# Kernel optimization log

Hardware: AMD Instinct MI355X
Metric: run time of the kernel (lower is better)

## Reference

```python
import jax, jax.numpy as jnp
from jax import lax
import numpy as np

D_MODEL = 96; D_STATE = 16; SSM_RATIO = 2.0; D_CONV = 3; K = 4
D_INNER = int(SSM_RATIO * D_MODEL)      # 192
DT_RANK = -(-D_MODEL // 16)             # ceil(96/16) = 6
B_SZ = 4; H = 32; W = 32

# ---- zig-zag (snake) index helpers (static numpy) ----
def _snake_h(Hh, Ww):
    idx = np.tile(np.arange(Ww), (Hh, 1)); idx[1::2] = idx[1::2, ::-1]; return idx  # (H,W)

def _snake_v(Hh, Ww):
    idx = np.tile(np.arange(Hh)[:, None], (1, Ww)); idx[:, 1::2] = idx[::-1, 1::2]; return idx  # (H,W)

def _h_scan(x, d):
    Hh, Ww = x.shape[-2:]
    if d == 'left':
        x = jnp.flip(x, (-1, -2))
    return x[:, :, np.arange(Hh)[:, None], _snake_h(Hh, Ww)]

def _v_scan(x, d):
    Bb, Cc, Hh, Ww = x.shape
    if d == 'up':
        x = jnp.flip(x, (-1, -2))
    t = x[:, :, _snake_v(Hh, Ww), np.arange(Ww)[None, :]]  # gather along H per column
    return jnp.swapaxes(t, -1, -2).reshape(Bb, Cc, Hh, Ww)

def _h_merge(x, d):
    Hh, Ww = x.shape[-2:]
    t = x[:, :, np.arange(Hh)[:, None], _snake_h(Hh, Ww)]
    if d == 'left':
        t = jnp.flip(t, (-1, -2))
    return t

def _v_merge(x, d):
    Hh, Ww = x.shape[-2:]
    t2 = jnp.swapaxes(x, -1, -2)  # (B,C,W,H); requires H==W like the torch source
    t = t2[:, :, _snake_v(Hh, Ww), np.arange(Ww)[None, :]]
    if d == 'up':
        t = jnp.flip(t, (-1, -2))
    return t

def cross_scan(x):
    return jnp.stack([_v_scan(x, 'down'), _v_scan(x, 'up'), _h_scan(x, 'right'), _h_scan(x, 'left')], axis=1)

def cross_merge(ys):
    return (_v_merge(ys[:, 0], 'down') + _v_merge(ys[:, 1], 'up')
            + _h_merge(ys[:, 2], 'right') + _h_merge(ys[:, 3], 'left'))

def selective_scan(u, delta, A, Bs, Cs, Dp, delta_bias):
    # u,delta:(B,K,D,L)  A:(K,D,N)  Bs,Cs:(B,K,N,L)  Dp,delta_bias:(K,D)
    delta = jax.nn.softplus(delta + delta_bias[None, :, :, None])
    dA = jnp.exp(jnp.einsum('bkdl,kdn->lbkdn', delta, A))
    dBu = jnp.einsum('bkdl,bkdl,bknl->lbkdn', delta, u, Bs)
    Ct = jnp.moveaxis(Cs, -1, 0)  # (L,B,K,N)
    def step(h, inp):
        dA_t, dBu_t, c_t = inp
        h = dA_t * h + dBu_t
        return h, jnp.einsum('bkdn,bkn->bkd', h, c_t)
    h0 = jnp.zeros(dA.shape[1:], u.dtype)
    _, ys = lax.scan(step, h0, (dA, dBu, Ct))
    return jnp.moveaxis(ys, 0, -1) + Dp[None, :, :, None] * u  # (B,K,D,L)

def setup_inputs() -> dict:
    key = jax.random.key(0)
    ks = jax.random.split(key, 8)
    x = jax.random.normal(ks[0], (B_SZ, D_MODEL, H, W), jnp.float32)
    in_proj_w = jax.random.normal(ks[1], (2 * D_INNER, D_MODEL), jnp.float32) * (D_MODEL ** -0.5)
    conv_w = jax.random.normal(ks[2], (D_INNER, 1, D_CONV, D_CONV), jnp.float32) * 0.2  # depthwise
    conv_b = jnp.zeros((D_INNER,), jnp.float32)
    x_proj_w = jax.random.normal(ks[3], (K, DT_RANK + 2 * D_STATE, D_INNER), jnp.float32) * (D_INNER ** -0.5)
    s = DT_RANK ** -0.5
    dt_w = jax.random.uniform(ks[4], (K, D_INNER, DT_RANK), jnp.float32, -s, s)
    dt = jax.random.uniform(ks[5], (K, D_INNER), jnp.float32, 0.001, 0.1)
    dt_b = jnp.log(jnp.expm1(dt))  # inverse softplus, as in dt_init
    A_logs = jnp.tile(jnp.log(jnp.arange(1, D_STATE + 1, dtype=jnp.float32)), (K * D_INNER, 1))
    Ds = jnp.ones((K * D_INNER,), jnp.float32)
    gn_gamma = jnp.ones((D_INNER,), jnp.float32)
    gn_beta = jnp.zeros((D_INNER,), jnp.float32)
    out_proj_w = jax.random.normal(ks[6], (D_MODEL, D_INNER), jnp.float32) * (D_INNER ** -0.5)
    return {'x': x, 'in_proj_w': in_proj_w, 'conv_w': conv_w, 'conv_b': conv_b,
            'x_proj_w': x_proj_w, 'dt_w': dt_w, 'dt_b': dt_b, 'A_logs': A_logs, 'Ds': Ds,
            'gn_gamma': gn_gamma, 'gn_beta': gn_beta, 'out_proj_w': out_proj_w}

def reference(x, in_proj_w, conv_w, conv_b, x_proj_w, dt_w, dt_b, A_logs, Ds, gn_gamma, gn_beta, out_proj_w):
    Bb, _, Hh, Ww = x.shape; L = Hh * Ww
    xz = jnp.einsum('bchw,oc->bohw', x, in_proj_w)          # in_proj (1x1 conv, no bias)
    xx, z = jnp.split(xz, 2, axis=1)
    z = jax.nn.silu(z)
    xx = lax.conv_general_dilated(xx, conv_w, (1, 1), 'SAME', feature_group_count=D_INNER,
                                  dimension_numbers=('NCHW', 'OIHW', 'NCHW')) + conv_b[None, :, None, None]
    xx = jax.nn.silu(xx)
    xs = cross_scan(xx).reshape(Bb, K, D_INNER, L)          # 4-direction zig-zag scan
    x_dbl = jnp.einsum('bkdl,kcd->bkcl', xs, x_proj_w)
    dts = jnp.einsum('bkrl,kdr->bkdl', x_dbl[:, :, :DT_RANK], dt_w)
    Bs = x_dbl[:, :, DT_RANK:DT_RANK + D_STATE]
    Cs = x_dbl[:, :, DT_RANK + D_STATE:]
    A = -jnp.exp(A_logs).reshape(K, D_INNER, D_STATE)
    y = selective_scan(xs, dts, A, Bs, Cs, Ds.reshape(K, D_INNER), dt_b)
    y = cross_merge(y.reshape(Bb, K, D_INNER, Hh, Ww))       # (B,D,H,W)
    # out_norm: GroupNorm(1, d_inner) == layernorm over (C,H,W) per sample
    mu = jnp.mean(y, axis=(1, 2, 3), keepdims=True)
    var = jnp.var(y, axis=(1, 2, 3), keepdims=True)
    y = (y - mu) * lax.rsqrt(var + 1e-6)
    y = y * gn_gamma[None, :, None, None] + gn_beta[None, :, None, None]
    y = y * z
    return jnp.einsum('bchw,oc->bohw', y, out_proj_w)
```

## Files before the change

### kernel.cpp

```cpp
#include <hip/hip_runtime.h>
#include <math.h>

#define Bsz 4
#define DM 96
#define DI 192
#define NS 16
#define RK 6
#define KK 4
#define HH 32
#define WW 32
#define LL 1024
#define NC 64
#define CS 16

__device__ __forceinline__ float silu_f(float x) { return x / (1.f + __expf(-x)); }

__device__ __forceinline__ int l_of_hw(int k, int h, int w) {
    if (k == 1 || k == 3) { h = 31 - h; w = 31 - w; }
    if (k < 2) return w * 32 + ((w & 1) ? 31 - h : h);
    return h * 32 + ((h & 1) ? 31 - w : w);
}

__global__ void in_proj_k(const float* __restrict__ x, const float* __restrict__ w,
                          float* __restrict__ xx, float* __restrict__ zs,
                          float* __restrict__ stats) {
    int bi = blockIdx.x;
    int t = threadIdx.x;
    if (bi == 0 && t < 2 * Bsz) stats[t] = 0.f;
    int lb = bi & 3;
    int og = (bi >> 2) % 48;
    int b = bi / 192;
    int l = lb * 256 + t;
    const float* xb = x + (size_t)b * DM * LL + l;
    float acc[8];
#pragma unroll
    for (int g = 0; g < 8; g++) acc[g] = 0.f;
    for (int c = 0; c < DM; c++) {
        float xv = xb[(size_t)c * LL];
#pragma unroll
        for (int g = 0; g < 8; g++)
            acc[g] = fmaf(xv, w[(size_t)(og * 8 + g) * DM + c], acc[g]);
    }
#pragma unroll
    for (int g = 0; g < 8; g++) {
        int o = og * 8 + g;
        if (o < DI) xx[((size_t)b * DI + o) * LL + l] = acc[g];
        else        zs[((size_t)b * DI + (o - DI)) * LL + l] = silu_f(acc[g]);
    }
}

__global__ void convxs_k(const float* __restrict__ xx, const float* __restrict__ cw,
                         const float* __restrict__ cb, float* __restrict__ xs) {
    __shared__ float tile[32][65];
    int bi = blockIdx.x;
    int h0 = bi % 32;
    int dt = (bi / 32) % 3;
    int b = bi / 96;
    int d0 = dt * 64;
    int t = threadIdx.x;
    int wi = t & 31, dg = t >> 5;

#pragma unroll
    for (int pass = 0; pass < 8; pass++) {
        int di = pass * 8 + dg;
        int d = d0 + di;
        const float* xp = xx + ((size_t)b * DI + d) * LL;
        const float* wp = cw + d * 9;
        float acc = cb[d];
#pragma unroll
        for (int kh = 0; kh < 3; kh++) {
            int hh = h0 + kh - 1;
            if (hh < 0 || hh >= HH) continue;
#pragma unroll
            for (int kw = 0; kw < 3; kw++) {
                int ww2 = wi + kw - 1;
                if (ww2 < 0 || ww2 >= WW) continue;
                acc = fmaf(xp[hh * WW + ww2], wp[kh * 3 + kw], acc);
            }
        }
        tile[wi][di] = silu_f(acc);
    }
    __syncthreads();

    int di = t & 63, hg = t >> 6;
#pragma unroll
    for (int k = 0; k < KK; k++) {
        float* xsk = xs + ((size_t)b * KK + k) * LL * DI;
#pragma unroll
        for (int rep = 0; rep < 8; rep++) {
            int w2 = rep * 4 + hg;
            int l = l_of_hw(k, h0, w2);
            xsk[(size_t)l * DI + d0 + di] = tile[w2][di];
        }
    }
}

__global__ void __launch_bounds__(512)
xdbl_k(const float* __restrict__ xs, const float* __restrict__ xpw,
       float* __restrict__ xdbl) {
    __shared__ float tile[64 * 193];
    int blk = blockIdx.x;
    int bk = blk >> 4, lt = blk & 15;
    int k = bk & 3;
    int t = threadIdx.x;

    const float4* src4 = (const float4*)(xs + ((size_t)bk * LL + lt * 64) * DI);
#pragma unroll
    for (int i = 0; i < 6; i++) {
        int j4 = t + i * 512;
        float4 v = src4[j4];
        int l = j4 / 48;
        int d = (j4 % 48) * 4;
        float* dst = &tile[l * 193 + d];
        dst[0] = v.x; dst[1] = v.y; dst[2] = v.z; dst[3] = v.w;
    }
    __syncthreads();

    int ll = t & 63;
    int cg = t >> 6;
    int c0 = cg * 5;
    int wlim = (c0 + 5 <= 38) ? 5 : (38 - c0);
    const float* wk = xpw + (size_t)k * 38 * DI;

    float acc[5];
#pragma unroll
    for (int j = 0; j < 5; j++) acc[j] = 0.f;
    const float* xrow = &tile[ll * 193];
#pragma unroll 4
    for (int d = 0; d < DI; d++) {
        float xv = xrow[d];
#pragma unroll
        for (int j = 0; j < 5; j++) {
            int cc = c0 + j; cc = (cc > 37) ? 37 : cc;
            acc[j] = fmaf(xv, wk[(size_t)cc * DI + d], acc[j]);
        }
    }
    float* orow = xdbl + ((size_t)bk * LL + lt * 64 + ll) * 38;
#pragma unroll
    for (int j = 0; j < 5; j++)
        if (j < wlim) orow[c0 + j] = acc[j];
}

__global__ void scan_p1(const float* __restrict__ xs, const float* __restrict__ xdbl,
                        const float* __restrict__ dtw_g, const float* __restrict__ dtb_g,
                        const float* __restrict__ Alog,
                        float* __restrict__ Pst, float* __restrict__ Hloc) {
    int blk = blockIdx.x;
    int bk = blk / NC, c = blk % NC;
    int k = bk & 3;
    int d = threadIdx.x;
    int kd = k * DI + d;

    float A[NS];
#pragma unroll
    for (int n = 0; n < NS; n++) A[n] = -__expf(Alog[(size_t)kd * NS + n]);
    float dtw[RK];
#pragma unroll
    for (int r = 0; r < RK; r++) dtw[r] = dtw_g[(size_t)kd * RK + r];
    float dtb = dtb_g[kd];

    float h[NS], P[NS];
#pragma unroll
    for (int n = 0; n < NS; n++) { h[n] = 0.f; P[n] = 1.f; }

    const float* xdbase = xdbl + ((size_t)bk * LL + c * CS) * 38;
    const float* xsbase = xs + ((size_t)bk * LL + c * CS) * DI;

    for (int s = 0; s < CS; s++) {
        const float* xd = xdbase + s * 38;
        float dt = dtb;
#pragma unroll
        for (int r = 0; r < RK; r++) dt = fmaf(xd[r], dtw[r], dt);
        dt = (dt > 20.f) ? dt : log1pf(__expf(dt));
        float du = dt * xsbase[(size_t)s * DI + d];
#pragma unroll
        for (int n = 0; n < NS; n++) {
            float a = __expf(dt * A[n]);
            h[n] = fmaf(a, h[n], du * xd[6 + n]);
            P[n] *= a;
        }
    }
    size_t base = ((size_t)blk * DI + d) * NS;
#pragma unroll
    for (int n = 0; n < NS; n++) { Pst[base + n] = P[n]; Hloc[base + n] = h[n]; }
}

__global__ void scan_mid(const float* __restrict__ Pst, float* __restrict__ Hloc) {
    int gid = blockIdx.x * 256 + threadIdx.x;
    int bk = gid / (DI * NS);
    int dn = gid % (DI * NS);
    size_t base = (size_t)bk * NC * DI * NS + dn;
    float h = 0.f;
    for (int c = 0; c < NC; c++) {
        size_t a = base + (size_t)c * DI * NS;
        float p = Pst[a];
        float loc = Hloc[a];
        Hloc[a] = h;
        h = fmaf(p, h, loc);
    }
}

__global__ void scan_p3(const float* __restrict__ xs, const float* __restrict__ xdbl,
                        const float* __restrict__ dtw_g, const float* __restrict__ dtb_g,
                        const float* __restrict__ Alog, const float* __restrict__ Ds,
                        const float* __restrict__ Hin, float* __restrict__ ys) {
    int blk = blockIdx.x;
    int bk = blk / NC, c = blk % NC;
    int k = bk & 3;
    int d = threadIdx.x;
    int kd = k * DI + d;

    float A[NS];
#pragma unroll
    for (int n = 0; n < NS; n++) A[n] = -__expf(Alog[(size_t)kd * NS + n]);
    float dtw[RK];
#pragma unroll
    for (int r = 0; r < RK; r++) dtw[r] = dtw_g[(size_t)kd * RK + r];
    float dtb = dtb_g[kd];
    float Dp = Ds[kd];

    float h[NS];
    size_t hbase = ((size_t)blk * DI + d) * NS;
#pragma unroll
    for (int n = 0; n < NS; n++) h[n] = Hin[hbase + n];

    const float* xdbase = xdbl + ((size_t)bk * LL + c * CS) * 38;
    const float* xsbase = xs + ((size_t)bk * LL + c * CS) * DI;
    float* ybase = ys + ((size_t)bk * LL + c * CS) * DI;

    for (int s = 0; s < CS; s++) {
        const float* xd = xdbase + s * 38;
        float dt = dtb;
#pragma unroll
        for (int r = 0; r < RK; r++) dt = fmaf(xd[r], dtw[r], dt);
        dt = (dt > 20.f) ? dt : log1pf(__expf(dt));
        float u = xsbase[(size_t)s * DI + d];
        float du = dt * u;
        float y = 0.f;
#pragma unroll
        for (int n = 0; n < NS; n++) {
            float a = __expf(dt * A[n]);
            h[n] = fmaf(a, h[n], du * xd[6 + n]);
            y = fmaf(h[n], xd[22 + n], y);
        }
        ybase[(size_t)s * DI + d] = fmaf(Dp, u, y);
    }
}

#define MT 16
__global__ void merge_k(const float* __restrict__ ys, float* __restrict__ ym,
                        float* __restrict__ stats) {
    __shared__ float tile[MT][DI + 1];
    __shared__ float sh1[3], sh2[3];
    int b = blockIdx.y;
    int hw0 = blockIdx.x * MT;
    int d = threadIdx.x;
    const float* yb = ys + (size_t)b * KK * LL * DI;

    float s1 = 0.f, s2 = 0.f;
#pragma unroll
    for (int hwi = 0; hwi < MT; hwi++) {
        int hw = hw0 + hwi;
        int h = hw >> 5, w = hw & 31;
        int l0 = l_of_hw(0, h, w);
        int l1 = l_of_hw(1, h, w);
        int l2 = l_of_hw(2, h, w);
        int l3 = l_of_hw(3, h, w);
        float v = yb[((size_t)0 * LL + l0) * DI + d]
                + yb[((size_t)1 * LL + l1) * DI + d]
                + yb[((size_t)2 * LL + l2) * DI + d]
                + yb[((size_t)3 * LL + l3) * DI + d];
        tile[hwi][d] = v;
        s1 += v; s2 = fmaf(v, v, s2);
    }
#pragma unroll
    for (int off = 32; off > 0; off >>= 1) {
        s1 += __shfl_down(s1, off);
        s2 += __shfl_down(s2, off);
    }
    int lane = threadIdx.x & 63, wid = threadIdx.x >> 6;
    if (lane == 0) { sh1[wid] = s1; sh2[wid] = s2; }
    __syncthreads();
    if (threadIdx.x == 0) {
        atomicAdd(&stats[b * 2],     sh1[0] + sh1[1] + sh1[2]);
        atomicAdd(&stats[b * 2 + 1], sh2[0] + sh2[1] + sh2[2]);
    }
#pragma unroll
    for (int rep = 0; rep < MT; rep++) {
        int j = rep * DI + threadIdx.x;
        int d2 = j >> 4;
        int hwi = j & (MT - 1);
        ym[((size_t)b * DI + d2) * LL + hw0 + hwi] = tile[hwi][d2];
    }
}

__global__ void yz_k(const float* __restrict__ ym, const float* __restrict__ zs,
                     const float* __restrict__ g, const float* __restrict__ be,
                     const float* __restrict__ stats, float* __restrict__ yz) {
    int idx = blockIdx.x * 256 + threadIdx.x;
    int c = (idx >> 10) % DI;
    int b = idx / (LL * DI);
    const float Ninv = 1.f / (float)(DI * LL);
    float mu = stats[b * 2] * Ninv;
    float var = stats[b * 2 + 1] * Ninv - mu * mu;
    float rstd = rsqrtf(var + 1e-6f);
    float v = (ym[idx] - mu) * rstd * g[c] + be[c];
    yz[idx] = v * zs[idx];
}

__global__ void out_k(const float* __restrict__ yz, const float* __restrict__ wo,
                      float* __restrict__ out) {
    int bi = blockIdx.x;
    int t = threadIdx.x;
    int lb = bi & 3;
    int og = (bi >> 2) % 24;
    int b = bi / 96;
    int l = lb * 256 + t;
    const float* yb = yz + (size_t)b * DI * LL + l;
    float acc[4];
#pragma unroll
    for (int g = 0; g < 4; g++) acc[g] = 0.f;
    for (int c = 0; c < DI; c++) {
        float yv = yb[(size_t)c * LL];
#pragma unroll
        for (int g = 0; g < 4; g++)
            acc[g] = fmaf(yv, wo[(size_t)(og * 4 + g) * DI + c], acc[g]);
    }
#pragma unroll
    for (int g = 0; g < 4; g++)
        out[((size_t)b * DM + og * 4 + g) * LL + l] = acc[g];
}

extern "C" void kernel_launch(void* const* d_in, const int* in_sizes, int n_in,
                              void* d_out, int out_size, void* d_ws, size_t ws_size,
                              hipStream_t stream) {
    const float* x    = (const float*)d_in[0];
    const float* ipw  = (const float*)d_in[1];
    const float* cw   = (const float*)d_in[2];
    const float* cb   = (const float*)d_in[3];
    const float* xpw  = (const float*)d_in[4];
    const float* dtw  = (const float*)d_in[5];
    const float* dtb  = (const float*)d_in[6];
    const float* Alog = (const float*)d_in[7];
    const float* Ds   = (const float*)d_in[8];
    const float* gng  = (const float*)d_in[9];
    const float* gnb  = (const float*)d_in[10];
    const float* opw  = (const float*)d_in[11];
    float* out = (float*)d_out;

    float* ws = (float*)d_ws;
    const size_t o_xx   = 0;
    const size_t o_zs   = o_xx + (size_t)Bsz * DI * LL;
    const size_t o_xs   = o_zs + (size_t)Bsz * DI * LL;
    const size_t o_xdbl = o_xs + (size_t)Bsz * KK * LL * DI;
    const size_t o_P    = o_xdbl + (size_t)Bsz * KK * LL * 38;
    const size_t o_H    = o_P + (size_t)Bsz * KK * NC * DI * NS;
    const size_t o_st   = o_H + (size_t)Bsz * KK * NC * DI * NS;

    float* xx    = ws + o_xx;
    float* zs    = ws + o_zs;
    float* xs    = ws + o_xs;
    float* xdbl  = ws + o_xdbl;
    float* Pst   = ws + o_P;
    float* Hst   = ws + o_H;
    float* stats = ws + o_st;
    float* ys = Pst;
    float* ym = xx;
    float* yz = Hst;

    hipLaunchKernelGGL(in_proj_k, dim3(768), dim3(256), 0, stream, x, ipw, xx, zs, stats);
    hipLaunchKernelGGL(convxs_k, dim3(384), dim3(256), 0, stream, xx, cw, cb, xs);
    hipLaunchKernelGGL(xdbl_k, dim3(256), dim3(512), 0, stream, xs, xpw, xdbl);
    hipLaunchKernelGGL(scan_p1, dim3(Bsz * KK * NC), dim3(192), 0, stream,
                       xs, xdbl, dtw, dtb, Alog, Pst, Hst);
    hipLaunchKernelGGL(scan_mid, dim3(192), dim3(256), 0, stream, Pst, Hst);
    hipLaunchKernelGGL(scan_p3, dim3(Bsz * KK * NC), dim3(192), 0, stream,
                       xs, xdbl, dtw, dtb, Alog, Ds, Hst, ys);
    hipLaunchKernelGGL(merge_k, dim3(LL / MT, Bsz), dim3(192), 0, stream, ys, ym, stats);
    hipLaunchKernelGGL(yz_k, dim3(3072), dim3(256), 0, stream, ym, zs, gng, gnb, stats, yz);
    hipLaunchKernelGGL(out_k, dim3(384), dim3(256), 0, stream, yz, opw, out);
}
```

Baseline: 233.7 us.

## Fuse all stages into one cooperative persistent kernel with grid syncs

Replaces the chain of nine kernel launches with a single cooperative kernel of 512 blocks that runs each stage in turn, separated by grid-wide barriers. Stages are re-partitioned to fit the fixed grid: in_proj computes 12 outputs per thread, xdbl streams xs through a smaller LDS slice, scan blocks each handle two chunks, and the yz normalisation is fused into the out-projection. The aim is to remove per-launch overhead and the intermediate yz round trip to memory. In exchange, several stages now run with fewer or idle threads, and each grid sync adds its own cost. The old multi-kernel path stays as a fallback if the cooperative launch fails.

```diff
diff --git a/kernel.cpp b/kernel.cpp
--- a/kernel.cpp
+++ b/kernel.cpp
@@ -1,5 +1,8 @@
 #include <hip/hip_runtime.h>
+#include <hip/hip_cooperative_groups.h>
 #include <math.h>
+
+namespace cg = cooperative_groups;
 
 #define Bsz 4
 #define DM 96
@@ -12,6 +15,7 @@
 #define LL 1024
 #define NC 64
 #define CS 16
+#define MT 8
 
 __device__ __forceinline__ float silu_f(float x) { return x / (1.f + __expf(-x)); }
 
@@ -19,6 +23,327 @@
     if (k == 1 || k == 3) { h = 31 - h; w = 31 - w; }
     if (k < 2) return w * 32 + ((w & 1) ? 31 - h : h);
     return h * 32 + ((h & 1) ? 31 - w : w);
+}
+
+#define O_XX   0
+#define O_ZS   (O_XX + Bsz * DI * LL)
+#define O_XS   (O_ZS + Bsz * DI * LL)
+#define O_XDBL (O_XS + Bsz * KK * LL * DI)
+#define O_P    (O_XDBL + Bsz * KK * LL * 38)
+#define O_H    (O_P + Bsz * KK * NC * DI * NS)
+#define O_ST   (O_H + Bsz * KK * NC * DI * NS)
+
+__global__ void __launch_bounds__(256, 2)
+mega_k(const float* __restrict__ x, const float* __restrict__ ipw,
+       const float* __restrict__ cw, const float* __restrict__ cb,
+       const float* __restrict__ xpw, const float* __restrict__ dtw_g,
+       const float* __restrict__ dtb_g, const float* __restrict__ Alog,
+       const float* __restrict__ Ds, const float* __restrict__ gng,
+       const float* __restrict__ gnb, const float* __restrict__ opw,
+       float* __restrict__ out, float* __restrict__ ws) {
+    cg::grid_group grid = cg::this_grid();
+    __shared__ float lds[3136];
+
+    float* xx    = ws + O_XX;
+    float* zs    = ws + O_ZS;
+    float* xs    = ws + O_XS;
+    float* xdbl  = ws + O_XDBL;
+    float* Pst   = ws + O_P;
+    float* Hst   = ws + O_H;
+    float* stats = ws + O_ST;
+    float* ys = Pst;
+    float* ym = xx;
+
+    int bi = blockIdx.x;
+    int t = threadIdx.x;
+
+    {
+        if (bi == 0 && t < 2 * Bsz) stats[t] = 0.f;
+        int b = bi / 128;
+        int rest = bi % 128;
+        int og = rest >> 2;
+        int lb = rest & 3;
+        int l = lb * 256 + t;
+        const float* xb = x + (size_t)b * DM * LL + l;
+        float acc[12];
+#pragma unroll
+        for (int g = 0; g < 12; g++) acc[g] = 0.f;
+        for (int c = 0; c < DM; c++) {
+            float xv = xb[(size_t)c * LL];
+#pragma unroll
+            for (int g = 0; g < 12; g++)
+                acc[g] = fmaf(xv, ipw[(size_t)(og * 12 + g) * DM + c], acc[g]);
+        }
+#pragma unroll
+        for (int g = 0; g < 12; g++) {
+            int o = og * 12 + g;
+            if (o < DI) xx[((size_t)b * DI + o) * LL + l] = acc[g];
+            else        zs[((size_t)b * DI + (o - DI)) * LL + l] = silu_f(acc[g]);
+        }
+    }
+    grid.sync();
+
+    if (bi < 384) {
+        float (*tile)[65] = (float(*)[65])lds;
+        int h0 = bi % 32;
+        int dt = (bi / 32) % 3;
+        int b = bi / 96;
+        int d0 = dt * 64;
+        int wi = t & 31, dg = t >> 5;
+#pragma unroll
+        for (int pass = 0; pass < 8; pass++) {
+            int di = pass * 8 + dg;
+            int d = d0 + di;
+            const float* xp = xx + ((size_t)b * DI + d) * LL;
+            const float* wp = cw + d * 9;
+            float acc = cb[d];
+#pragma unroll
+            for (int kh = 0; kh < 3; kh++) {
+                int hh = h0 + kh - 1;
+                if (hh < 0 || hh >= HH) continue;
+#pragma unroll
+                for (int kw = 0; kw < 3; kw++) {
+                    int ww2 = wi + kw - 1;
+                    if (ww2 < 0 || ww2 >= WW) continue;
+                    acc = fmaf(xp[hh * WW + ww2], wp[kh * 3 + kw], acc);
+                }
+            }
+            tile[wi][di] = silu_f(acc);
+        }
+        __syncthreads();
+        int di = t & 63, hg = t >> 6;
+#pragma unroll
+        for (int k = 0; k < KK; k++) {
+            float* xsk = xs + ((size_t)b * KK + k) * LL * DI;
+#pragma unroll
+            for (int rep = 0; rep < 8; rep++) {
+                int w2 = rep * 4 + hg;
+                int l = l_of_hw(k, h0, w2);
+                xsk[(size_t)l * DI + d0 + di] = tile[w2][di];
+            }
+        }
+    }
+    grid.sync();
+
+    if (bi < 256) {
+        int bk = bi >> 4, lt = bi & 15;
+        int k = bk & 3;
+        int ll = t & 63;
+        int cgp = t >> 6;
+        int c0 = cgp * 10;
+        int wlim = 38 - c0; if (wlim > 10) wlim = 10;
+        const float* wk = xpw + (size_t)k * 38 * DI;
+        const float4* src4 = (const float4*)(xs + ((size_t)bk * LL + lt * 64) * DI);
+        float acc[10];
+#pragma unroll
+        for (int j = 0; j < 10; j++) acc[j] = 0.f;
+#pragma unroll
+        for (int sl = 0; sl < 4; sl++) {
+            __syncthreads();
+#pragma unroll
+            for (int i = 0; i < 3; i++) {
+                int j = t + i * 256;
+                int l = j / 12;
+                int c4 = j % 12;
+                float4 v = src4[(size_t)l * 48 + sl * 12 + c4];
+                float* dst = &lds[l * 49 + c4 * 4];
+                dst[0] = v.x; dst[1] = v.y; dst[2] = v.z; dst[3] = v.w;
+            }
+            __syncthreads();
+            const float* xrow = &lds[ll * 49];
+            const float* wks = wk + sl * 48;
+#pragma unroll 4
+            for (int dd = 0; dd < 48; dd++) {
+                float xv = xrow[dd];
+#pragma unroll
+                for (int j = 0; j < 10; j++) {
+                    int cc = c0 + j; cc = (cc > 37) ? 37 : cc;
+                    acc[j] = fmaf(xv, wks[(size_t)cc * DI + dd], acc[j]);
+                }
+            }
+        }
+        float* orow = xdbl + ((size_t)bk * LL + lt * 64 + ll) * 38;
+#pragma unroll
+        for (int j = 0; j < 10; j++)
+            if (j < wlim) orow[c0 + j] = acc[j];
+    }
+    grid.sync();
+
+    if (t < 192) {
+        int d = t;
+#pragma unroll
+        for (int rep = 0; rep < 2; rep++) {
+            int unit = bi * 2 + rep;
+            int bk = unit / NC, c = unit % NC;
+            int k = bk & 3;
+            int kd = k * DI + d;
+            float A[NS];
+#pragma unroll
+            for (int n = 0; n < NS; n++) A[n] = -__expf(Alog[(size_t)kd * NS + n]);
+            float dtw[RK];
+#pragma unroll
+            for (int r = 0; r < RK; r++) dtw[r] = dtw_g[(size_t)kd * RK + r];
+            float dtb = dtb_g[kd];
+            float h[NS], P[NS];
+#pragma unroll
+            for (int n = 0; n < NS; n++) { h[n] = 0.f; P[n] = 1.f; }
+            const float* xdbase = xdbl + ((size_t)bk * LL + c * CS) * 38;
+            const float* xsbase = xs + ((size_t)bk * LL + c * CS) * DI;
+            for (int s = 0; s < CS; s++) {
+                const float* xd = xdbase + s * 38;
+                float dt = dtb;
+#pragma unroll
+                for (int r = 0; r < RK; r++) dt = fmaf(xd[r], dtw[r], dt);
+                dt = (dt > 20.f) ? dt : log1pf(__expf(dt));
+                float du = dt * xsbase[(size_t)s * DI + d];
+#pragma unroll
+                for (int n = 0; n < NS; n++) {
+                    float a = __expf(dt * A[n]);
+                    h[n] = fmaf(a, h[n], du * xd[6 + n]);
+                    P[n] *= a;
+                }
+            }
+            size_t base = ((size_t)unit * DI + d) * NS;
+#pragma unroll
+            for (int n = 0; n < NS; n++) { Pst[base + n] = P[n]; Hst[base + n] = h[n]; }
+        }
+    }
+    grid.sync();
+
+    {
+        int g = bi * 256 + t;
+        if (g < Bsz * KK * DI * NS) {
+            int bk = g / (DI * NS);
+            int dn = g % (DI * NS);
+            size_t base = (size_t)bk * NC * DI * NS + dn;
+            float h = 0.f;
+            for (int c = 0; c < NC; c++) {
+                size_t a = base + (size_t)c * DI * NS;
+                float p = Pst[a];
+                float loc = Hst[a];
+                Hst[a] = h;
+                h = fmaf(p, h, loc);
+            }
+        }
+    }
+    grid.sync();
+
+    if (t < 192) {
+        int d = t;
+#pragma unroll
+        for (int rep = 0; rep < 2; rep++) {
+            int unit = bi * 2 + rep;
+            int bk = unit / NC, c = unit % NC;
+            int k = bk & 3;
+            int kd = k * DI + d;
+            float A[NS];
+#pragma unroll
+            for (int n = 0; n < NS; n++) A[n] = -__expf(Alog[(size_t)kd * NS + n]);
+            float dtw[RK];
+#pragma unroll
+            for (int r = 0; r < RK; r++) dtw[r] = dtw_g[(size_t)kd * RK + r];
+            float dtb = dtb_g[kd];
+            float Dp = Ds[kd];
+            float h[NS];
+            size_t hbase = ((size_t)unit * DI + d) * NS;
+#pragma unroll
+            for (int n = 0; n < NS; n++) h[n] = Hst[hbase + n];
+            const float* xdbase = xdbl + ((size_t)bk * LL + c * CS) * 38;
+            const float* xsbase = xs + ((size_t)bk * LL + c * CS) * DI;
+            float* ybase = ys + ((size_t)bk * LL + c * CS) * DI;
+            for (int s = 0; s < CS; s++) {
+                const float* xd = xdbase + s * 38;
+                float dt = dtb;
+#pragma unroll
+                for (int r = 0; r < RK; r++) dt = fmaf(xd[r], dtw[r], dt);
+                dt = (dt > 20.f) ? dt : log1pf(__expf(dt));
+                float u = xsbase[(size_t)s * DI + d];
+                float du = dt * u;
+                float y = 0.f;
+#pragma unroll
+                for (int n = 0; n < NS; n++) {
+                    float a = __expf(dt * A[n]);
+                    h[n] = fmaf(a, h[n], du * xd[6 + n]);
+                    y = fmaf(h[n], xd[22 + n], y);
+                }
+                ybase[(size_t)s * DI + d] = fmaf(Dp, u, y);
+            }
+        }
+    }
+    grid.sync();
+
+    {
+        float (*mtile)[193] = (float(*)[193])lds;
+        float* sh1 = lds + MT * 193;
+        float* sh2 = sh1 + 4;
+        int b = bi >> 7;
+        int hw0 = (bi & 127) * MT;
+        const float* yb = ys + (size_t)b * KK * LL * DI;
+        float s1 = 0.f, s2 = 0.f;
+        if (t < DI) {
+            int d = t;
+#pragma unroll
+            for (int hwi = 0; hwi < MT; hwi++) {
+                int hw = hw0 + hwi;
+                int h = hw >> 5, w = hw & 31;
+                float v = yb[((size_t)0 * LL + l_of_hw(0, h, w)) * DI + d]
+                        + yb[((size_t)1 * LL + l_of_hw(1, h, w)) * DI + d]
+                        + yb[((size_t)2 * LL + l_of_hw(2, h, w)) * DI + d]
+                        + yb[((size_t)3 * LL + l_of_hw(3, h, w)) * DI + d];
+                mtile[hwi][d] = v;
+                s1 += v; s2 = fmaf(v, v, s2);
+            }
+#pragma unroll
+            for (int off = 32; off > 0; off >>= 1) {
+                s1 += __shfl_down(s1, off);
+                s2 += __shfl_down(s2, off);
+            }
+            int lane = t & 63, wid = t >> 6;
+            if (lane == 0) { sh1[wid] = s1; sh2[wid] = s2; }
+        }
+        __syncthreads();
+        if (t == 0) {
+            atomicAdd(&stats[b * 2],     sh1[0] + sh1[1] + sh1[2]);
+            atomicAdd(&stats[b * 2 + 1], sh2[0] + sh2[1] + sh2[2]);
+        }
+        if (t < DI) {
+#pragma unroll
+            for (int rep = 0; rep < MT; rep++) {
+                int j = rep * DI + t;
+                int d2 = j >> 3;
+                int hwi = j & (MT - 1);
+                ym[((size_t)b * DI + d2) * LL + hw0 + hwi] = mtile[hwi][d2];
+            }
+        }
+    }
+    grid.sync();
+
+    {
+        int b = bi / 128;
+        int rest = bi % 128;
+        int og = rest >> 2;
+        int lb = rest & 3;
+        int l = lb * 256 + t;
+        int o3 = og * 3;
+        const float Ninv = 1.f / (float)(DI * LL);
+        float mu = stats[b * 2] * Ninv;
+        float var = stats[b * 2 + 1] * Ninv - mu * mu;
+        float rstd = rsqrtf(var + 1e-6f);
+        float a0 = 0.f, a1 = 0.f, a2 = 0.f;
+        const float* ymb = ym + (size_t)b * DI * LL + l;
+        const float* zsb = zs + (size_t)b * DI * LL + l;
+        for (int c = 0; c < DI; c++) {
+            float ymv = ymb[(size_t)c * LL];
+            float zv  = zsb[(size_t)c * LL];
+            float yzv = fmaf((ymv - mu) * rstd, gng[c], gnb[c]) * zv;
+            a0 = fmaf(yzv, opw[(size_t)(o3 + 0) * DI + c], a0);
+            a1 = fmaf(yzv, opw[(size_t)(o3 + 1) * DI + c], a1);
+            a2 = fmaf(yzv, opw[(size_t)(o3 + 2) * DI + c], a2);
+        }
+        out[((size_t)b * DM + o3 + 0) * LL + l] = a0;
+        out[((size_t)b * DM + o3 + 1) * LL + l] = a1;
+        out[((size_t)b * DM + o3 + 2) * LL + l] = a2;
+    }
 }
 
 __global__ void in_proj_k(const float* __restrict__ x, const float* __restrict__ w,
@@ -59,7 +384,6 @@
     int d0 = dt * 64;
     int t = threadIdx.x;
     int wi = t & 31, dg = t >> 5;
-
 #pragma unroll
     for (int pass = 0; pass < 8; pass++) {
         int di = pass * 8 + dg;
@@ -81,7 +405,6 @@
         tile[wi][di] = silu_f(acc);
     }
     __syncthreads();
-
     int di = t & 63, hg = t >> 6;
 #pragma unroll
     for (int k = 0; k < KK; k++) {
@@ -103,7 +426,6 @@
     int bk = blk >> 4, lt = blk & 15;
     int k = bk & 3;
     int t = threadIdx.x;
-
     const float4* src4 = (const float4*)(xs + ((size_t)bk * LL + lt * 64) * DI);
 #pragma unroll
     for (int i = 0; i < 6; i++) {
@@ -115,13 +437,11 @@
         dst[0] = v.x; dst[1] = v.y; dst[2] = v.z; dst[3] = v.w;
     }
     __syncthreads();
-
     int ll = t & 63;
-    int cg = t >> 6;
-    int c0 = cg * 5;
+    int cg2 = t >> 6;
+    int c0 = cg2 * 5;
     int wlim = (c0 + 5 <= 38) ? 5 : (38 - c0);
     const float* wk = xpw + (size_t)k * 38 * DI;
-
     float acc[5];
 #pragma unroll
     for (int j = 0; j < 5; j++) acc[j] = 0.f;
@@ -150,7 +470,6 @@
     int k = bk & 3;
     int d = threadIdx.x;
     int kd = k * DI + d;
-
     float A[NS];
 #pragma unroll
     for (int n = 0; n < NS; n++) A[n] = -__expf(Alog[(size_t)kd * NS + n]);
@@ -158,14 +477,11 @@
 #pragma unroll
     for (int r = 0; r < RK; r++) dtw[r] = dtw_g[(size_t)kd * RK + r];
     float dtb = dtb_g[kd];
-
     float h[NS], P[NS];
 #pragma unroll
     for (int n = 0; n < NS; n++) { h[n] = 0.f; P[n] = 1.f; }
-
     const float* xdbase = xdbl + ((size_t)bk * LL + c * CS) * 38;
     const float* xsbase = xs + ((size_t)bk * LL + c * CS) * DI;
-
     for (int s = 0; s < CS; s++) {
         const float* xd = xdbase + s * 38;
         float dt = dtb;
@@ -209,7 +525,6 @@
     int k = bk & 3;
     int d = threadIdx.x;
     int kd = k * DI + d;
-
     float A[NS];
 #pragma unroll
     for (int n = 0; n < NS; n++) A[n] = -__expf(Alog[(size_t)kd * NS + n]);
@@ -218,16 +533,13 @@
     for (int r = 0; r < RK; r++) dtw[r] = dtw_g[(size_t)kd * RK + r];
     float dtb = dtb_g[kd];
     float Dp = Ds[kd];
-
     float h[NS];
     size_t hbase = ((size_t)blk * DI + d) * NS;
 #pragma unroll
     for (int n = 0; n < NS; n++) h[n] = Hin[hbase + n];
-
     const float* xdbase = xdbl + ((size_t)bk * LL + c * CS) * 38;
     const float* xsbase = xs + ((size_t)bk * LL + c * CS) * DI;
     float* ybase = ys + ((size_t)bk * LL + c * CS) * DI;
-
     for (int s = 0; s < CS; s++) {
         const float* xd = xdbase + s * 38;
         float dt = dtb;
@@ -247,29 +559,24 @@
     }
 }
 
-#define MT 16
+#define MTF 16
 __global__ void merge_k(const float* __restrict__ ys, float* __restrict__ ym,
                         float* __restrict__ stats) {
-    __shared__ float tile[MT][DI + 1];
+    __shared__ float tile[MTF][DI + 1];
     __shared__ float sh1[3], sh2[3];
     int b = blockIdx.y;
-    int hw0 = blockIdx.x * MT;
+    int hw0 = blockIdx.x * MTF;
     int d = threadIdx.x;
     const float* yb = ys + (size_t)b * KK * LL * DI;
-
     float s1 = 0.f, s2 = 0.f;
 #pragma unroll
-    for (int hwi = 0; hwi < MT; hwi++) {
+    for (int hwi = 0; hwi < MTF; hwi++) {
         int hw = hw0 + hwi;
         int h = hw >> 5, w = hw & 31;
-        int l0 = l_of_hw(0, h, w);
-        int l1 = l_of_hw(1, h, w);
-        int l2 = l_of_hw(2, h, w);
-        int l3 = l_of_hw(3, h, w);
-        float v = yb[((size_t)0 * LL + l0) * DI + d]
-                + yb[((size_t)1 * LL + l1) * DI + d]
-                + yb[((size_t)2 * LL + l2) * DI + d]
-                + yb[((size_t)3 * LL + l3) * DI + d];
+        float v = yb[((size_t)0 * LL + l_of_hw(0, h, w)) * DI + d]
+                + yb[((size_t)1 * LL + l_of_hw(1, h, w)) * DI + d]
+                + yb[((size_t)2 * LL + l_of_hw(2, h, w)) * DI + d]
+                + yb[((size_t)3 * LL + l_of_hw(3, h, w)) * DI + d];
         tile[hwi][d] = v;
         s1 += v; s2 = fmaf(v, v, s2);
     }
@@ -286,10 +593,10 @@
         atomicAdd(&stats[b * 2 + 1], sh2[0] + sh2[1] + sh2[2]);
     }
 #pragma unroll
-    for (int rep = 0; rep < MT; rep++) {
+    for (int rep = 0; rep < MTF; rep++) {
         int j = rep * DI + threadIdx.x;
         int d2 = j >> 4;
-        int hwi = j & (MT - 1);
+        int hwi = j & (MTF - 1);
         ym[((size_t)b * DI + d2) * LL + hw0 + hwi] = tile[hwi][d2];
     }
 }
@@ -347,36 +654,34 @@
     const float* gnb  = (const float*)d_in[10];
     const float* opw  = (const float*)d_in[11];
     float* out = (float*)d_out;
-
     float* ws = (float*)d_ws;
-    const size_t o_xx   = 0;
-    const size_t o_zs   = o_xx + (size_t)Bsz * DI * LL;
-    const size_t o_xs   = o_zs + (size_t)Bsz * DI * LL;
-    const size_t o_xdbl = o_xs + (size_t)Bsz * KK * LL * DI;
-    const size_t o_P    = o_xdbl + (size_t)Bsz * KK * LL * 38;
-    const size_t o_H    = o_P + (size_t)Bsz * KK * NC * DI * NS;
-    const size_t o_st   = o_H + (size_t)Bsz * KK * NC * DI * NS;
-
-    float* xx    = ws + o_xx;
-    float* zs    = ws + o_zs;
-    float* xs    = ws + o_xs;
-    float* xdbl  = ws + o_xdbl;
-    float* Pst   = ws + o_P;
-    float* Hst   = ws + o_H;
-    float* stats = ws + o_st;
-    float* ys = Pst;
-    float* ym = xx;
-    float* yz = Hst;
-
-    hipLaunchKernelGGL(in_proj_k, dim3(768), dim3(256), 0, stream, x, ipw, xx, zs, stats);
-    hipLaunchKernelGGL(convxs_k, dim3(384), dim3(256), 0, stream, xx, cw, cb, xs);
-    hipLaunchKernelGGL(xdbl_k, dim3(256), dim3(512), 0, stream, xs, xpw, xdbl);
-    hipLaunchKernelGGL(scan_p1, dim3(Bsz * KK * NC), dim3(192), 0, stream,
-                       xs, xdbl, dtw, dtb, Alog, Pst, Hst);
-    hipLaunchKernelGGL(scan_mid, dim3(192), dim3(256), 0, stream, Pst, Hst);
-    hipLaunchKernelGGL(scan_p3, dim3(Bsz * KK * NC), dim3(192), 0, stream,
-                       xs, xdbl, dtw, dtb, Alog, Ds, Hst, ys);
-    hipLaunchKernelGGL(merge_k, dim3(LL / MT, Bsz), dim3(192), 0, stream, ys, ym, stats);
-    hipLaunchKernelGGL(yz_k, dim3(3072), dim3(256), 0, stream, ym, zs, gng, gnb, stats, yz);
-    hipLaunchKernelGGL(out_k, dim3(384), dim3(256), 0, stream, yz, opw, out);
-}
+
+    void* args[] = {&x, &ipw, &cw, &cb, &xpw, &dtw, &dtb, &Alog, &Ds,
+                    &gng, &gnb, &opw, &out, &ws};
+    hipError_t st = hipLaunchCooperativeKernel((void*)mega_k, dim3(512), dim3(256),
+                                               args, 0, stream);
+    if (st != hipSuccess) {
+        (void)hipGetLastError();
+        float* xx    = ws + O_XX;
+        float* zs    = ws + O_ZS;
+        float* xs    = ws + O_XS;
+        float* xdbl  = ws + O_XDBL;
+        float* Pst   = ws + O_P;
+        float* Hst   = ws + O_H;
+        float* stats = ws + O_ST;
+        float* ys = Pst;
+        float* ym = xx;
+        float* yz = Hst;
+        hipLaunchKernelGGL(in_proj_k, dim3(768), dim3(256), 0, stream, x, ipw, xx, zs, stats);
+        hipLaunchKernelGGL(convxs_k, dim3(384), dim3(256), 0, stream, xx, cw, cb, xs);
+        hipLaunchKernelGGL(xdbl_k, dim3(256), dim3(512), 0, stream, xs, xpw, xdbl);
+        hipLaunchKernelGGL(scan_p1, dim3(Bsz * KK * NC), dim3(192), 0, stream,
+                           xs, xdbl, dtw, dtb, Alog, Pst, Hst);
+        hipLaunchKernelGGL(scan_mid, dim3(192), dim3(256), 0, stream, Pst, Hst);
+        hipLaunchKernelGGL(scan_p3, dim3(Bsz * KK * NC), dim3(192), 0, stream,
+                           xs, xdbl, dtw, dtb, Alog, Ds, Hst, ys);
+        hipLaunchKernelGGL(merge_k, dim3(LL / MTF, Bsz), dim3(192), 0, stream, ys, ym, stats);
+        hipLaunchKernelGGL(yz_k, dim3(3072), dim3(256), 0, stream, ym, zs, gng, gnb, stats, yz);
+        hipLaunchKernelGGL(out_k, dim3(384), dim3(256), 0, stream, yz, opw, out);
+    }
+}
```

Result: slower. 705.2 us (+201.7%).
